# Performance work log

Hardware: AMD Instinct MI355X
Metric: run time of the kernel (lower is better)

## Reference

```python
import jax, jax.numpy as jnp
import numpy as np

N = 10000
E = 320000
F_IN = 256
HID = 64
HEADS = 8
NUM_CLASSES = 2
NEG_SLOPE = 0.2


def _glorot(key, shape):
    fan_in, fan_out = shape[0], shape[-1]
    lim = (6.0 / (fan_in + fan_out)) ** 0.5
    return jax.random.uniform(key, shape, jnp.float32, -lim, lim)


def setup_inputs() -> dict:
    key = jax.random.key(0)
    ks = jax.random.split(key, 20)
    x = jax.random.normal(ks[0], (N, F_IN), jnp.float32)
    edge_index = jax.random.randint(ks[1], (2, E), 0, N, jnp.int64)
    d = {
        "x": x,
        "edge_index": edge_index,
        # layer 1: in=256 -> heads=8, C=64, concat -> 512
        "W1": _glorot(ks[2], (F_IN, HEADS * HID)),
        "a_src1": _glorot(ks[3], (HEADS, HID)),
        "a_dst1": _glorot(ks[4], (HEADS, HID)),
        "b1": jnp.zeros((HEADS * HID,), jnp.float32),
        # layer 2: in=512 -> heads=8, C=64, concat -> 512
        "W2": _glorot(ks[5], (HEADS * HID, HEADS * HID)),
        "a_src2": _glorot(ks[6], (HEADS, HID)),
        "a_dst2": _glorot(ks[7], (HEADS, HID)),
        "b2": jnp.zeros((HEADS * HID,), jnp.float32),
        # output conv: in=512 -> heads=1, C=64, no concat
        "W3": _glorot(ks[8], (HEADS * HID, HID)),
        "a_src3": _glorot(ks[9], (1, HID)),
        "a_dst3": _glorot(ks[10], (1, HID)),
        "b3": jnp.zeros((HID,), jnp.float32),
        # classifier
        "lin_W": _glorot(ks[11], (HID, NUM_CLASSES)),
        "lin_b": jnp.zeros((NUM_CLASSES,), jnp.float32),
    }
    return d


def _gat_layer(x, src, dst, W, a_src, a_dst, b, heads, ch, concat):
    # project: [N, H, C]
    h = (x @ W).reshape(-1, heads, ch)
    alpha_src = jnp.sum(h * a_src, axis=-1)  # [N, H]
    alpha_dst = jnp.sum(h * a_dst, axis=-1)  # [N, H]
    # per-edge attention logits (edge j -> i uses src alpha of j, dst alpha of i)
    e = jax.nn.leaky_relu(alpha_src[src] + alpha_dst[dst], NEG_SLOPE)  # [E, H]
    # segment softmax over incoming edges of each destination node
    m = jax.ops.segment_max(e, dst, num_segments=N)  # [N, H]
    m = jnp.where(jnp.isfinite(m), m, 0.0)
    ex = jnp.exp(e - m[dst])
    denom = jax.ops.segment_sum(ex, dst, num_segments=N)
    alpha = ex / (denom[dst] + 1e-16)  # [E, H]
    # weighted message aggregation
    out = jax.ops.segment_sum(h[src] * alpha[:, :, None], dst, num_segments=N)  # [N, H, C]
    if concat:
        out = out.reshape(N, heads * ch)
    else:
        out = out.mean(axis=1)
    return out + b


def reference(x, edge_index, W1, a_src1, a_dst1, b1, W2, a_src2, a_dst2, b2,
              W3, a_src3, a_dst3, b3, lin_W, lin_b):
    # PyG GATConv adds self loops by default
    loop = jnp.arange(N, dtype=edge_index.dtype)
    src = jnp.concatenate([edge_index[0], loop])
    dst = jnp.concatenate([edge_index[1], loop])

    h = _gat_layer(x, src, dst, W1, a_src1, a_dst1, b1, HEADS, HID, True)
    h = jax.nn.elu(h)
    h = _gat_layer(h, src, dst, W2, a_src2, a_dst2, b2, HEADS, HID, True)
    h = jax.nn.elu(h)
    h = _gat_layer(h, src, dst, W3, a_src3, a_dst3, b3, 1, HID, False)
    logits = h @ lin_W + lin_b
    return jax.nn.log_softmax(logits, axis=1)
```

## Files before the change

### kernel.cpp

```cpp
#include <hip/hip_runtime.h>
#include <cmath>

#define NEG 0.2f

typedef __bf16 bf16x8 __attribute__((ext_vector_type(8)));
typedef float  f32x4  __attribute__((ext_vector_type(4)));

__device__ __forceinline__ void async16(const __bf16* g, __bf16* l) {
  __builtin_amdgcn_global_load_lds(
      (const __attribute__((address_space(1))) void*)g,
      (__attribute__((address_space(3))) void*)l, 16, 0, 0);
}
__device__ __forceinline__ f32x4 mfma16(bf16x8 a, bf16x8 b, f32x4 c) {
  return __builtin_amdgcn_mfma_f32_16x16x32_bf16(a, b, c, 0, 0, 0);
}

__global__ void count_kernel(const int* __restrict__ ei, int* __restrict__ counts, int E, int Nn) {
  int e = blockIdx.x * blockDim.x + threadIdx.x;
  if (e >= E + Nn) return;
  int d = (e < E) ? ei[E + e] : (e - E);
  atomicAdd(&counts[d], 1);
}

__global__ __launch_bounds__(1024) void scan_kernel(const int* __restrict__ counts,
                                                    int* __restrict__ row_ptr,
                                                    int* __restrict__ cursor,
                                                    int n, int total) {
  __shared__ int sums[1024];
  int t = threadIdx.x;
  int per = (n + 1023) >> 10;
  int base = t * per;
  int s = 0;
  for (int i = 0; i < per; ++i) { int idx = base + i; if (idx < n) s += counts[idx]; }
  sums[t] = s;
  __syncthreads();
  for (int st = 1; st < 1024; st <<= 1) {
    int v = (t >= st) ? sums[t - st] : 0;
    __syncthreads();
    sums[t] += v;
    __syncthreads();
  }
  int off = (t == 0) ? 0 : sums[t - 1];
  for (int i = 0; i < per; ++i) {
    int idx = base + i;
    if (idx < n) { row_ptr[idx] = off; cursor[idx] = off; off += counts[idx]; }
  }
  if (t == 0) row_ptr[n] = total;
}

__global__ void scatter_kernel(const int* __restrict__ ei, int* __restrict__ cursor,
                               int* __restrict__ src_sorted, int E, int Nn) {
  int e = blockIdx.x * blockDim.x + threadIdx.x;
  if (e >= E + Nn) return;
  int s, d;
  if (e < E) { s = ei[e]; d = ei[E + e]; } else { s = e - E; d = e - E; }
  int pos = atomicAdd(&cursor[d], 1);
  src_sorted[pos] = s;
}

__global__ void prep_kernel(const float* __restrict__ x, __bf16* __restrict__ xsh,
                            __bf16* __restrict__ xsl,
                            const float* __restrict__ W1, __bf16* __restrict__ W1th,
                            const float* __restrict__ W2, __bf16* __restrict__ W2th,
                            const float* __restrict__ W3, __bf16* __restrict__ W3th,
                            int* __restrict__ counts, int Nn) {
  int i = blockIdx.x * blockDim.x + threadIdx.x;
  if (i < Nn) { counts[i] = 0; return; }
  i -= Nn;
  int nx = Nn * 256;
  if (i < nx) {
    float v = x[i];
    __bf16 h = (__bf16)v;
    xsh[i] = h;
    xsl[i] = (__bf16)(v - (float)h);
    return;
  }
  i -= nx;
  if (i < 256 * 512) {
    int k = i / 512, c = i % 512;
    W1th[(size_t)c * 256 + k] = (__bf16)W1[i];
    return;
  }
  i -= 256 * 512;
  if (i < 512 * 512) {
    int k = i / 512, c = i % 512;
    W2th[(size_t)c * 512 + k] = (__bf16)W2[i];
    return;
  }
  i -= 512 * 512;
  if (i < 512 * 64) {
    int k = i / 64, c = i % 64;
    W3th[(size_t)c * 512 + k] = (__bf16)W3[i];
    return;
  }
}

template <bool ASPLIT>
__global__ __launch_bounds__(256, 4) void gemm_v3(
    const __bf16* __restrict__ Ah, const __bf16* __restrict__ Al,
    const __bf16* __restrict__ Bth,
    __bf16* __restrict__ Cb,
    const float* __restrict__ asrc, const float* __restrict__ adst,
    float* __restrict__ als, float* __restrict__ ald,
    int M, int K, int Nc, int PX) {
  __shared__ __bf16 sAh[64 * 64], sBh[128 * 64];
  __shared__ __bf16 sAl[ASPLIT ? 64 * 64 : 64];

  int p = blockIdx.x;
  int c = p & 7, j = p >> 3;
  int x = c * PX + (j >> 2);
  int y = j & 3;
  int rowBase = x * 64, colBase = y * 128;
  if (rowBase >= M) return;

  int tid = threadIdx.x;
  int lane = tid & 63, wave = tid >> 6;
  int r16 = lane & 15, koct = lane >> 4, msk = r16 & 7;

  int fa0 = tid, fa1 = 256 + tid;
  int ar0 = fa0 >> 3, ar1 = fa1 >> 3;
  int as0 = (fa0 & 7) ^ (ar0 & 7);
  int as1 = (fa1 & 7) ^ (ar1 & 7);
  size_t aoff0 = (size_t)min(rowBase + ar0, M - 1) * K + as0 * 8;
  size_t aoff1 = (size_t)min(rowBase + ar1, M - 1) * K + as1 * 8;
  size_t boff[4];
#pragma unroll
  for (int r = 0; r < 4; ++r) {
    int f = r * 256 + tid;
    int col = f >> 3;
    int s = (f & 7) ^ (col & 7);
    boff[r] = (size_t)(colBase + col) * K + s * 8;
  }
  int lb0 = (wave * 64) * 8;
  int lb1 = ((256 + wave * 64)) * 8;
  int lb2 = ((512 + wave * 64)) * 8;
  int lb3 = ((768 + wave * 64)) * 8;

  int arow = wave * 16 + r16;
  f32x4 acc[8] = {};

  for (int k0 = 0; k0 < K; k0 += 64) {
    __syncthreads();
    async16(Ah + aoff0 + k0, sAh + lb0);
    async16(Ah + aoff1 + k0, sAh + lb1);
    if (ASPLIT) {
      async16(Al + aoff0 + k0, sAl + lb0);
      async16(Al + aoff1 + k0, sAl + lb1);
    }
    async16(Bth + boff[0] + k0, sBh + lb0);
    async16(Bth + boff[1] + k0, sBh + lb1);
    async16(Bth + boff[2] + k0, sBh + lb2);
    async16(Bth + boff[3] + k0, sBh + lb3);
    __syncthreads();

#pragma unroll
    for (int kk = 0; kk < 2; ++kk) {
      int ks = ((kk * 4 + koct) ^ msk) * 8;
      bf16x8 ah = *reinterpret_cast<const bf16x8*>(sAh + arow * 64 + ks);
      bf16x8 al;
      if (ASPLIT) al = *reinterpret_cast<const bf16x8*>(sAl + arow * 64 + ks);
      bf16x8 bh[8];
#pragma unroll
      for (int fn = 0; fn < 8; ++fn)
        bh[fn] = *reinterpret_cast<const bf16x8*>(sBh + (fn * 16 + r16) * 64 + ks);
#pragma unroll
      for (int fn = 0; fn < 8; ++fn) {
        acc[fn] = mfma16(ah, bh[fn], acc[fn]);
        if (ASPLIT) acc[fn] = mfma16(al, bh[fn], acc[fn]);
      }
    }
  }

  float asv[8], adv[8];
#pragma unroll
  for (int fn = 0; fn < 8; ++fn) {
    int ai = (y * 2 + (fn >> 2)) * 64 + (fn & 3) * 16 + r16;
    asv[fn] = asrc[ai];
    adv[fn] = adst[ai];
  }
#pragma unroll
  for (int r = 0; r < 4; ++r) {
    int row = rowBase + wave * 16 + koct * 4 + r;
    float psA = 0.f, pdA = 0.f, psB = 0.f, pdB = 0.f;
#pragma unroll
    for (int fn = 0; fn < 8; ++fn) {
      float v = acc[fn][r];
      if (row < M) Cb[(size_t)row * Nc + colBase + fn * 16 + r16] = (__bf16)v;
      if (fn < 4) { psA = fmaf(v, asv[fn], psA); pdA = fmaf(v, adv[fn], pdA); }
      else        { psB = fmaf(v, asv[fn], psB); pdB = fmaf(v, adv[fn], pdB); }
    }
#pragma unroll
    for (int sft = 1; sft < 16; sft <<= 1) {
      psA += __shfl_xor(psA, sft); pdA += __shfl_xor(pdA, sft);
      psB += __shfl_xor(psB, sft); pdB += __shfl_xor(pdB, sft);
    }
    if (r16 == 0 && row < M) {
      als[(size_t)row * 8 + y * 2 + 0] = psA;
      ald[(size_t)row * 8 + y * 2 + 0] = pdA;
      als[(size_t)row * 8 + y * 2 + 1] = psB;
      ald[(size_t)row * 8 + y * 2 + 1] = pdB;
    }
  }
}

__global__ __launch_bounds__(256, 4) void gemm_v2(
    const __bf16* __restrict__ Ah,
    const __bf16* __restrict__ Bth,
    float* __restrict__ Cf,
    const float* __restrict__ asrc, const float* __restrict__ adst,
    float* __restrict__ als, float* __restrict__ ald,
    int M, int K, int Nc) {
  __shared__ __bf16 sAh[128 * 64], sBh[64 * 64];

  int x = blockIdx.x;
  int rowBase = x * 128, colBase = 0;
  if (rowBase >= M) return;

  int tid = threadIdx.x;
  int lane = tid & 63, wave = tid >> 6;
  int r16 = lane & 15, koct = lane >> 4, msk = r16 & 7;

  f32x4 acc[2][4] = {};

  for (int k0 = 0; k0 < K; k0 += 64) {
    __syncthreads();
#pragma unroll
    for (int r = 0; r < 4; ++r) {
      int flat = r * 256 + tid;
      int row = flat >> 3;
      int grow = rowBase + row;
      if (grow >= M) grow = M - 1;
      int s = (flat & 7) ^ (row & 7);
      size_t go = (size_t)grow * K + k0 + s * 8;
      int lb = (r * 256 + wave * 64) * 8;
      async16(Ah + go, sAh + lb);
    }
#pragma unroll
    for (int r = 0; r < 2; ++r) {
      int flat = r * 256 + tid;
      int col = flat >> 3;
      int s = (flat & 7) ^ (col & 7);
      size_t go = (size_t)(colBase + col) * K + k0 + s * 8;
      int lb = (r * 256 + wave * 64) * 8;
      async16(Bth + go, sBh + lb);
    }
    __syncthreads();

#pragma unroll
    for (int kk = 0; kk < 2; ++kk) {
      bf16x8 ah[2], bh[4];
#pragma unroll
      for (int fm = 0; fm < 2; ++fm) {
        int off = (wave * 32 + fm * 16 + r16) * 64 + (((kk * 4 + koct) ^ msk) * 8);
        ah[fm] = *reinterpret_cast<const bf16x8*>(sAh + off);
      }
#pragma unroll
      for (int fn = 0; fn < 4; ++fn) {
        int off = (fn * 16 + r16) * 64 + (((kk * 4 + koct) ^ msk) * 8);
        bh[fn] = *reinterpret_cast<const bf16x8*>(sBh + off);
      }
#pragma unroll
      for (int fm = 0; fm < 2; ++fm)
#pragma unroll
        for (int fn = 0; fn < 4; ++fn)
          acc[fm][fn] = mfma16(ah[fm], bh[fn], acc[fm][fn]);
    }
  }

  float asv[4], adv[4];
#pragma unroll
  for (int fn = 0; fn < 4; ++fn) {
    asv[fn] = asrc[fn * 16 + r16];
    adv[fn] = adst[fn * 16 + r16];
  }
#pragma unroll
  for (int fm = 0; fm < 2; ++fm)
#pragma unroll
    for (int r = 0; r < 4; ++r) {
      int row = rowBase + wave * 32 + fm * 16 + koct * 4 + r;
      float ps = 0.f, pd = 0.f;
#pragma unroll
      for (int fn = 0; fn < 4; ++fn) {
        float v = acc[fm][fn][r];
        ps = fmaf(v, asv[fn], ps);
        pd = fmaf(v, adv[fn], pd);
        if (row < M) Cf[(size_t)row * Nc + fn * 16 + r16] = v;
      }
#pragma unroll
      for (int sft = 1; sft < 16; sft <<= 1) {
        ps += __shfl_xor(ps, sft);
        pd += __shfl_xor(pd, sft);
      }
      if (r16 == 0 && row < M) {
        als[row] = ps;
        ald[row] = pd;
      }
    }
}

__global__ __launch_bounds__(256) void agg8s_kernel(const __bf16* __restrict__ Hb,
                                                    const float* __restrict__ als,
                                                    const float* __restrict__ ald,
                                                    const float* __restrict__ bias,
                                                    const int* __restrict__ row_ptr,
                                                    const int* __restrict__ src_sorted,
                                                    __bf16* __restrict__ Oh,
                                                    int Nn) {
  int head = blockIdx.x & 7;
  int n = (blockIdx.x >> 3) * 4 + (threadIdx.x >> 6);
  if (n >= Nn) return;
  int lane = threadIdx.x & 63;
  int slot = lane >> 3, cg = lane & 7;
  int start = row_ptr[n], deg = row_ptr[n + 1] - start;
  float aldn = ald[n * 8 + head];
  const __bf16* hcol = Hb + head * 64 + cg * 8;

  float acc[8] = {};
  float ssum = 0.f;
  for (int e0 = 0; e0 < deg; e0 += 8) {
    int idx = src_sorted[start + min(e0 + slot, deg - 1)];
    float l = als[idx * 8 + head] + aldn;
    l = l > 0.f ? l : NEG * l;
    float w = (e0 + slot < deg) ? __expf(fminf(l, 80.f)) : 0.f;
    bf16x8 v = *reinterpret_cast<const bf16x8*>(hcol + (size_t)idx * 512);
    ssum += w;
#pragma unroll
    for (int j = 0; j < 8; ++j) acc[j] = fmaf(w, (float)v[j], acc[j]);
  }
#pragma unroll
  for (int s = 8; s < 64; s <<= 1) {
    ssum += __shfl_xor(ssum, s);
#pragma unroll
    for (int j = 0; j < 8; ++j) acc[j] += __shfl_xor(acc[j], s);
  }
  if (slot == 0) {
    float inv = 1.f / (ssum + 1e-16f);
    bf16x8 vh;
#pragma unroll
    for (int j = 0; j < 8; ++j) {
      float v = acc[j] * inv + bias[head * 64 + cg * 8 + j];
      v = v > 0.f ? v : expm1f(v);
      vh[j] = (__bf16)v;
    }
    *reinterpret_cast<bf16x8*>(Oh + (size_t)n * 512 + head * 64 + cg * 8) = vh;
  }
}

__global__ __launch_bounds__(256) void agg8_kernel(const __bf16* __restrict__ Hb,
                                                   const float* __restrict__ als,
                                                   const float* __restrict__ ald,
                                                   const float* __restrict__ bias,
                                                   const int* __restrict__ row_ptr,
                                                   const int* __restrict__ src_sorted,
                                                   __bf16* __restrict__ Oh,
                                                   int Nn) {
  int n = (blockIdx.x * 256 + threadIdx.x) >> 6;
  if (n >= Nn) return;
  int lane = threadIdx.x & 63;
  int hh = lane >> 3;
  int start = row_ptr[n], deg = row_ptr[n + 1] - start;
  float aldn = ald[n * 8 + hh];

  float acc[8] = {};
  float ssum = 0.f;
  float mrun = 0.f;
  const __bf16* hcol = Hb + lane * 8;
  for (int e0 = 0; e0 < deg; e0 += 8) {
    int idx[8];
    float lv[8];
    bf16x8 v[8];
#pragma unroll
    for (int i = 0; i < 8; ++i) {
      int e = e0 + i;
      if (e > deg - 1) e = deg - 1;
      idx[i] = src_sorted[start + e];
    }
#pragma unroll
    for (int i = 0; i < 8; ++i) lv[i] = als[idx[i] * 8 + hh];
#pragma unroll
    for (int i = 0; i < 8; ++i)
      v[i] = *reinterpret_cast<const bf16x8*>(hcol + (size_t)idx[i] * 512);
    float lm = -INFINITY;
#pragma unroll
    for (int i = 0; i < 8; ++i) {
      float l = lv[i] + aldn;
      l = l > 0.f ? l : NEG * l;
      lv[i] = l;
      lm = fmaxf(lm, l);
    }
    if (__builtin_expect(lm > mrun + 24.f, 0)) {
      float sc = __expf(mrun - lm);
      ssum *= sc;
#pragma unroll
      for (int j = 0; j < 8; ++j) acc[j] *= sc;
      mrun = lm;
    }
#pragma unroll
    for (int i = 0; i < 8; ++i) {
      float w = (e0 + i < deg) ? __expf(lv[i] - mrun) : 0.f;
      ssum += w;
#pragma unroll
      for (int j = 0; j < 8; ++j) acc[j] = fmaf(w, (float)v[i][j], acc[j]);
    }
  }

  float inv = 1.f / (ssum + 1e-16f);
  bf16x8 vh;
#pragma unroll
  for (int j = 0; j < 8; ++j) {
    float v = acc[j] * inv + bias[lane * 8 + j];
    v = v > 0.f ? v : expm1f(v);
    vh[j] = (__bf16)v;
  }
  *reinterpret_cast<bf16x8*>(Oh + (size_t)n * 512 + lane * 8) = vh;
}

__global__ __launch_bounds__(256) void agg1cls_kernel(const float* __restrict__ Hf,
                                                      const float* __restrict__ als,
                                                      const float* __restrict__ ald,
                                                      const float* __restrict__ bias,
                                                      const int* __restrict__ row_ptr,
                                                      const int* __restrict__ src_sorted,
                                                      const float* __restrict__ lw,
                                                      const float* __restrict__ lb,
                                                      float* __restrict__ out,
                                                      int Nn) {
  int n = (blockIdx.x * 256 + threadIdx.x) >> 6;
  if (n >= Nn) return;
  int lane = threadIdx.x & 63;
  int start = row_ptr[n], deg = row_ptr[n + 1] - start;
  float aldn = ald[n];

  float acc = 0.f, ssum = 0.f, mrun = 0.f;
  for (int e0 = 0; e0 < deg; e0 += 8) {
    int idx[8];
    float lv[8], hv[8];
#pragma unroll
    for (int i = 0; i < 8; ++i) {
      int e = e0 + i;
      if (e > deg - 1) e = deg - 1;
      idx[i] = src_sorted[start + e];
    }
#pragma unroll
    for (int i = 0; i < 8; ++i) lv[i] = als[idx[i]];
#pragma unroll
    for (int i = 0; i < 8; ++i) hv[i] = Hf[(size_t)idx[i] * 64 + lane];
    float lm = -INFINITY;
#pragma unroll
    for (int i = 0; i < 8; ++i) {
      float l = lv[i] + aldn;
      l = l > 0.f ? l : NEG * l;
      lv[i] = l;
      lm = fmaxf(lm, l);
    }
    if (__builtin_expect(lm > mrun + 24.f, 0)) {
      float sc = __expf(mrun - lm);
      ssum *= sc;
      acc *= sc;
      mrun = lm;
    }
#pragma unroll
    for (int i = 0; i < 8; ++i) {
      float w = (e0 + i < deg) ? __expf(lv[i] - mrun) : 0.f;
      ssum += w;
      acc = fmaf(w, hv[i], acc);
    }
  }
  float o = acc / (ssum + 1e-16f) + bias[lane];

  float p0 = o * lw[lane * 2 + 0];
  float p1 = o * lw[lane * 2 + 1];
  for (int s = 32; s; s >>= 1) {
    p0 += __shfl_xor(p0, s);
    p1 += __shfl_xor(p1, s);
  }
  if (lane == 0) {
    p0 += lb[0];
    p1 += lb[1];
    float mx = fmaxf(p0, p1);
    float lse = mx + logf(expf(p0 - mx) + expf(p1 - mx));
    out[n * 2 + 0] = p0 - lse;
    out[n * 2 + 1] = p1 - lse;
  }
}

extern "C" void kernel_launch(void* const* d_in, const int* in_sizes, int n_in,
                              void* d_out, int out_size, void* d_ws, size_t ws_size,
                              hipStream_t stream) {
  (void)n_in; (void)out_size; (void)ws_size;
  const float* x     = (const float*)d_in[0];
  const int*   ei    = (const int*)d_in[1];
  const float* W1    = (const float*)d_in[2];
  const float* asrc1 = (const float*)d_in[3];
  const float* adst1 = (const float*)d_in[4];
  const float* b1    = (const float*)d_in[5];
  const float* W2    = (const float*)d_in[6];
  const float* asrc2 = (const float*)d_in[7];
  const float* adst2 = (const float*)d_in[8];
  const float* b2    = (const float*)d_in[9];
  const float* W3    = (const float*)d_in[10];
  const float* asrc3 = (const float*)d_in[11];
  const float* adst3 = (const float*)d_in[12];
  const float* b3    = (const float*)d_in[13];
  const float* linW  = (const float*)d_in[14];
  const float* linb  = (const float*)d_in[15];
  float* out = (float*)d_out;

  int Nn = in_sizes[0] / 256;
  int E  = in_sizes[1] / 2;
  int E2 = E + Nn;

  char* w = (char*)d_ws;
  auto carve = [&](size_t bytes) {
    char* p = w;
    w += (bytes + 63) & ~(size_t)63;
    return p;
  };
  __bf16* xsh  = (__bf16*)carve((size_t)Nn * 256 * 2);
  __bf16* xsl  = (__bf16*)carve((size_t)Nn * 256 * 2);
  __bf16* Ahb  = (__bf16*)carve((size_t)Nn * 512 * 2);
  __bf16* Hb16 = (__bf16*)carve((size_t)Nn * 512 * 2);
  float*  Hb3  = (float*)carve((size_t)Nn * 64 * 4);
  float*  als  = (float*)carve((size_t)Nn * 8 * 4);
  float*  ald  = (float*)carve((size_t)Nn * 8 * 4);
  __bf16* W1th = (__bf16*)carve(256 * 512 * 2);
  __bf16* W2th = (__bf16*)carve(512 * 512 * 2);
  __bf16* W3th = (__bf16*)carve(512 * 64 * 2);
  int* counts     = (int*)carve((size_t)Nn * 4);
  int* cursor     = (int*)carve((size_t)Nn * 4);
  int* row_ptr    = (int*)carve(((size_t)Nn + 1) * 4);
  int* src_sorted = (int*)carve((size_t)E2 * 4);

  int prep_total = Nn + Nn * 256 + 256 * 512 + 512 * 512 + 512 * 64;
  prep_kernel<<<(prep_total + 255) / 256, 256, 0, stream>>>(
      x, xsh, xsl, W1, W1th, W2, W2th, W3, W3th, counts, Nn);
  count_kernel<<<(E2 + 255) / 256, 256, 0, stream>>>(ei, counts, E, Nn);
  scan_kernel<<<1, 1024, 0, stream>>>(counts, row_ptr, cursor, Nn, E2);
  scatter_kernel<<<(E2 + 255) / 256, 256, 0, stream>>>(ei, cursor, src_sorted, E, Nn);

  int gx64 = (Nn + 63) / 64;
  int PX3 = (gx64 + 7) / 8;
  int nblk3 = 8 * PX3 * 4;
  int gx128 = (Nn + 127) / 128;
  int ga = (Nn + 3) / 4;
  int gs = ga * 8;

  gemm_v3<true><<<nblk3, 256, 0, stream>>>(xsh, xsl, W1th, Hb16,
                                           asrc1, adst1, als, ald, Nn, 256, 512, PX3);
  agg8s_kernel<<<gs, 256, 0, stream>>>(Hb16, als, ald, b1, row_ptr, src_sorted, Ahb, Nn);
  gemm_v3<false><<<nblk3, 256, 0, stream>>>(Ahb, nullptr, W2th, Hb16,
                                            asrc2, adst2, als, ald, Nn, 512, 512, PX3);
  agg8_kernel<<<ga, 256, 0, stream>>>(Hb16, als, ald, b2, row_ptr, src_sorted, Ahb, Nn);
  gemm_v2<<<gx128, 256, 0, stream>>>(Ahb, W3th, Hb3,
                                     asrc3, adst3, als, ald, Nn, 512, 64);
  agg1cls_kernel<<<ga, 256, 0, stream>>>(Hb3, als, ald, b3, row_ptr, src_sorted,
                                         linW, linb, out, Nn);
}
```

Measured before the change: 232.6 us.

## Restructure layer-1 aggregation: per-lane edge batching with online softmax rescale

Replaces the layer-1 aggregation kernel. Each lane now walks all edges of one node for a 2-head slice, with 16 lanes covering 128 columns and 4 nodes per wave. It issues 8 index, logit and feature loads up front to raise memory-level parallelism, and drops the cross-slot shuffle reduction. A running-max rescale, applied only when the max jumps by more than 24, keeps exp from overflowing in place of the fixed clamp at 80. The cost is load imbalance, since lanes in a wave loop to the largest degree among their 4 nodes, plus extra register pressure from the 8 buffered bf16x8 vectors.

```diff
diff --git a/kernel.cpp b/kernel.cpp
--- a/kernel.cpp
+++ b/kernel.cpp
@@ -298,51 +298,85 @@
     }
 }
 
-__global__ __launch_bounds__(256) void agg8s_kernel(const __bf16* __restrict__ Hb,
-                                                    const float* __restrict__ als,
-                                                    const float* __restrict__ ald,
-                                                    const float* __restrict__ bias,
-                                                    const int* __restrict__ row_ptr,
-                                                    const int* __restrict__ src_sorted,
-                                                    __bf16* __restrict__ Oh,
-                                                    int Nn) {
-  int head = blockIdx.x & 7;
-  int n = (blockIdx.x >> 3) * 4 + (threadIdx.x >> 6);
-  if (n >= Nn) return;
-  int lane = threadIdx.x & 63;
-  int slot = lane >> 3, cg = lane & 7;
+__global__ __launch_bounds__(256) void agg8v4_kernel(const __bf16* __restrict__ Hb,
+                                                     const float* __restrict__ als,
+                                                     const float* __restrict__ ald,
+                                                     const float* __restrict__ bias,
+                                                     const int* __restrict__ row_ptr,
+                                                     const int* __restrict__ src_sorted,
+                                                     __bf16* __restrict__ Oh,
+                                                     int Nn) {
+  int c8 = blockIdx.x & 7;
+  int sl = c8 >> 1;
+  int chunk = (blockIdx.x >> 3) * 2 + (c8 & 1);
+  int lane = threadIdx.x & 63, wave = threadIdx.x >> 6;
+  int sub = lane >> 4;
+  int cg = lane & 15;
+  int n = chunk * 16 + wave * 4 + sub;
+  bool alive = (n < Nn);
+  if (!alive) n = Nn - 1;
+  int head = sl * 2 + (cg >> 3);
+  int colb = head * 64 + (cg & 7) * 8;
+
   int start = row_ptr[n], deg = row_ptr[n + 1] - start;
   float aldn = ald[n * 8 + head];
-  const __bf16* hcol = Hb + head * 64 + cg * 8;
+  int dm = deg;
+  dm = max(dm, __shfl_xor(dm, 16));
+  dm = max(dm, __shfl_xor(dm, 32));
 
   float acc[8] = {};
   float ssum = 0.f;
-  for (int e0 = 0; e0 < deg; e0 += 8) {
-    int idx = src_sorted[start + min(e0 + slot, deg - 1)];
-    float l = als[idx * 8 + head] + aldn;
-    l = l > 0.f ? l : NEG * l;
-    float w = (e0 + slot < deg) ? __expf(fminf(l, 80.f)) : 0.f;
-    bf16x8 v = *reinterpret_cast<const bf16x8*>(hcol + (size_t)idx * 512);
-    ssum += w;
-#pragma unroll
-    for (int j = 0; j < 8; ++j) acc[j] = fmaf(w, (float)v[j], acc[j]);
-  }
-#pragma unroll
-  for (int s = 8; s < 64; s <<= 1) {
-    ssum += __shfl_xor(ssum, s);
-#pragma unroll
-    for (int j = 0; j < 8; ++j) acc[j] += __shfl_xor(acc[j], s);
-  }
-  if (slot == 0) {
+  float mrun = 0.f;
+  const __bf16* hcol = Hb + colb;
+  for (int e0 = 0; e0 < dm; e0 += 8) {
+    int idx[8];
+    float lv[8];
+    bf16x8 v[8];
+#pragma unroll
+    for (int i = 0; i < 8; ++i) {
+      int e = e0 + i;
+      if (e > deg - 1) e = deg - 1;
+      idx[i] = src_sorted[start + e];
+    }
+#pragma unroll
+    for (int i = 0; i < 8; ++i) lv[i] = als[idx[i] * 8 + head];
+#pragma unroll
+    for (int i = 0; i < 8; ++i)
+      v[i] = *reinterpret_cast<const bf16x8*>(hcol + (size_t)idx[i] * 512);
+    float lm = -INFINITY;
+#pragma unroll
+    for (int i = 0; i < 8; ++i) {
+      float l = lv[i] + aldn;
+      l = l > 0.f ? l : NEG * l;
+      lv[i] = l;
+      lm = fmaxf(lm, l);
+    }
+    if (__builtin_expect(lm > mrun + 24.f, 0)) {
+      float sc = __expf(mrun - lm);
+      ssum *= sc;
+#pragma unroll
+      for (int j = 0; j < 8; ++j) acc[j] *= sc;
+      mrun = lm;
+    }
+#pragma unroll
+    for (int i = 0; i < 8; ++i) {
+      float w = (e0 + i < deg) ? __expf(lv[i] - mrun) : 0.f;
+      ssum += w;
+#pragma unroll
+      for (int j = 0; j < 8; ++j) acc[j] = fmaf(w, (float)v[i][j], acc[j]);
+    }
+  }
+
+  if (alive) {
     float inv = 1.f / (ssum + 1e-16f);
     bf16x8 vh;
 #pragma unroll
     for (int j = 0; j < 8; ++j) {
-      float v = acc[j] * inv + bias[head * 64 + cg * 8 + j];
+      float v = acc[j] * inv + bias[colb + j];
       v = v > 0.f ? v : expm1f(v);
       vh[j] = (__bf16)v;
     }
-    *reinterpret_cast<bf16x8*>(Oh + (size_t)n * 512 + head * 64 + cg * 8) = vh;
+    *reinterpret_cast<bf16x8*>(Oh + (size_t)n * 512 + colb) = vh;
   }
 }
 
@@ -543,11 +577,11 @@
   int nblk3 = 8 * PX3 * 4;
   int gx128 = (Nn + 127) / 128;
   int ga = (Nn + 3) / 4;
-  int gs = ga * 8;
+  int gv4 = ((Nn + 31) / 32) * 8;
 
   gemm_v3<true><<<nblk3, 256, 0, stream>>>(xsh, xsl, W1th, Hb16,
                                            asrc1, adst1, als, ald, Nn, 256, 512, PX3);
-  agg8s_kernel<<<gs, 256, 0, stream>>>(Hb16, als, ald, b1, row_ptr, src_sorted, Ahb, Nn);
+  agg8v4_kernel<<<gv4, 256, 0, stream>>>(Hb16, als, ald, b1, row_ptr, src_sorted, Ahb, Nn);
   gemm_v3<false><<<nblk3, 256, 0, stream>>>(Ahb, nullptr, W2th, Hb16,
                                             asrc2, adst2, als, ald, Nn, 512, 512, PX3);
   agg8_kernel<<<ga, 256, 0, stream>>>(Hb16, als, ald, b2, row_ptr, src_sorted, Ahb, Nn);
```

After: 202.8 us. 1.15x faster.
